# Performance work log

Measured on AMD Instinct MI355X. Metric: run time of the kernel, lower is better.

## Reference

```python
import jax, jax.numpy as jnp
import numpy as np

SEQ, SUB, B, V = 32, 16, 512, 258
U = SEQ // SUB
Z, CH, CO, DH = 512, 1024, 512, 1024


def _lstm_cell(x, h, c, Wi, Wh, bi, bh):
    # torch gate order: input, forget, cell, output
    g = x @ Wi + h @ Wh + bi + bh  # [B, 4H]
    i, f, gg, o = jnp.split(g, 4, axis=-1)
    c = jax.nn.sigmoid(f) * c + jax.nn.sigmoid(i) * jnp.tanh(gg)
    h = jax.nn.sigmoid(o) * jnp.tanh(c)
    return h, c


def _lstm2(xs, h1_0, p1, p2):
    # xs: [T,B,in]; h1_0: [B,H] layer-1 initial hidden.
    # Layer-2 hidden and both cell states start at zero (initialize_state in torch code).
    z0 = jnp.zeros_like(h1_0)
    def step(carry, x):
        h1, c1, h2, c2 = carry
        h1, c1 = _lstm_cell(x, h1, c1, *p1)
        h2, c2 = _lstm_cell(h1, h2, c2, *p2)
        return (h1, c1, h2, c2), h2
    _, hs = jax.lax.scan(step, (h1_0, z0, z0, z0), xs)
    return hs  # [T,B,H] top-layer hidden states


def setup_inputs() -> dict:
    key = jax.random.key(0)
    ks = iter(jax.random.split(key, 40))
    def w(shape, s=0.05):
        return jax.random.normal(next(ks), shape, dtype=jnp.float32) * s
    return {
        "z": jax.random.normal(next(ks), (B, Z), dtype=jnp.float32),
        "x": jax.random.uniform(next(ks), (SEQ, B, V), dtype=jnp.float32),
        "conductor_input": w((1, B, V)),
        "ci_W": w((Z, CH)), "ci_b": w((CH,)),
        "cW1i": w((V, 4 * CH)), "cW1h": w((CH, 4 * CH)), "cb1i": w((4 * CH,)), "cb1h": w((4 * CH,)),
        "cW2i": w((CH, 4 * CH)), "cW2h": w((CH, 4 * CH)), "cb2i": w((4 * CH,)), "cb2h": w((4 * CH,)),
        "co_W": w((CH, CO)), "co_b": w((CO,)),
        "di_W": w((CO, DH)), "di_b": w((DH,)),
        "dW1i": w((CO + V, 4 * DH)), "dW1h": w((DH, 4 * DH)), "db1i": w((4 * DH,)), "db1h": w((4 * DH,)),
        "dW2i": w((DH, 4 * DH)), "dW2h": w((DH, 4 * DH)), "db2i": w((4 * DH,)), "db2h": w((4 * DH,)),
        "fc_W": w((DH, V)), "fc_b": w((V,)),
    }


def reference(z, x, conductor_input, ci_W, ci_b, cW1i, cW1h, cb1i, cb1h, cW2i, cW2h, cb2i, cb2h, co_W, co_b, di_W, di_b, dW1i, dW1h, db1i, db1h, dW2i, dW2h, db2i, db2h, fc_W, fc_b):
    # --- conductor: 2-layer LSTM over U steps of a learned constant input ---
    h1 = jnp.tanh(z @ ci_W + ci_b)  # [B,CH] layer-1 init hidden
    cin = jnp.broadcast_to(conductor_input, (U, B, V))
    ch = _lstm2(cin, h1, (cW1i, cW1h, cb1i, cb1h), (cW2i, cW2h, cb2i, cb2h))  # [U,B,CH]
    c = ch @ co_W + co_b  # [U,B,CO]
    # --- decoder (teacher forcing): state resets each sub-sequence, so the U
    # segments of length SUB are independent given c -> vmap over segments ---
    sos = jnp.zeros((1, B, V), jnp.float32).at[:, :, 0].set(1.0)
    prev = jnp.concatenate([sos, x[:-1]], axis=0).reshape(U, SUB, B, V)
    cb = jnp.broadcast_to(c[:, None], (U, SUB, B, CO))
    dec_in = jnp.concatenate([cb, prev], axis=-1)  # [U,SUB,B,CO+V]
    def run_seg(xs, cj):
        h1_0 = jnp.tanh(cj @ di_W + di_b)  # [B,DH]
        return _lstm2(xs, h1_0, (dW1i, dW1h, db1i, db1h), (dW2i, dW2h, db2i, db2h))
    hs = jax.vmap(run_seg)(dec_in, c)  # [U,SUB,B,DH]
    logp = jax.nn.log_softmax(hs @ fc_W + fc_b, axis=-1)  # log(softmax(.)) fused
    return logp.reshape(SEQ, B, V).transpose(1, 0, 2)  # [B,SEQ,V]
```

## Files before the change

kernel.cpp:

```cpp
#include <hip/hip_runtime.h>
#include <cstddef>
#include <cstdint>


namespace {

typedef short s8v __attribute__((ext_vector_type(8)));
typedef float f4v __attribute__((ext_vector_type(4)));
typedef unsigned short ushort_t;

__device__ inline unsigned short f2bf(float f) {
    union { float f; unsigned u; } v; v.f = f;
    unsigned r = v.u + 0x7fff + ((v.u >> 16) & 1);
    return (unsigned short)(r >> 16);
}
__device__ inline float bf2f(ushort_t u) {
    union { unsigned u; float f; } v; v.u = ((unsigned)u) << 16; return v.f;
}
__device__ inline float sigm_f(float x) { return 1.f / (1.f + __expf(-x)); }
__device__ inline float tanh_f(float x) {
    const float e = __expf(2.f * fabsf(x));
    return copysignf(1.f - 2.f / (e + 1.f), x);
}

#define GLOAD_LDS(gp, lp)                                              \
    __builtin_amdgcn_global_load_lds(                                  \
        (const __attribute__((address_space(1))) void*)(gp),           \
        (__attribute__((address_space(3))) void*)(lp), 16, 0, 0)

__device__ __forceinline__ void gemm_core(
    const ushort_t* __restrict__ A1a, const ushort_t* __restrict__ A1b,
    int lda1, int K1, const ushort_t* __restrict__ B1t,
    const ushort_t* __restrict__ A2, int lda2, int K2,
    const ushort_t* __restrict__ B2t,
    int bm, int bn, ushort_t* lds, f4v acc[4][4])
{
    const int tid = threadIdx.x;
    const int wid = tid >> 6;
    const int lane = tid & 63;

    const int sr0 = wid * 16 + (lane >> 2);
    const int sr1 = sr0 + 64;
    const int rl0 = sr0 ^ ((sr0 >> 2) & 1);
    const int rl1 = sr1 ^ ((sr1 >> 2) & 1);
    const int c0 = (((lane & 3) ^ (rl0 & 3)) << 3);
    const int c1 = (((lane & 3) ^ (rl1 & 3)) << 3);
    const int ldst = wid * 512;

    auto arow = [&](const ushort_t* Aa, const ushort_t* Ab, int lda,
                    int r) -> const ushort_t* {
        return (Ab != nullptr && r >= 512) ? Ab + (size_t)(r - 512) * lda
                                           : Aa + (size_t)r * lda;
    };
    const ushort_t* a0 = arow(A1a, A1b, lda1, bm + rl0) + c0;
    const ushort_t* a1 = arow(A1a, A1b, lda1, bm + rl1) + c1;
    const ushort_t* b0 = B1t + (size_t)(bn + rl0) * K1 + c0;
    const ushort_t* b1 = B1t + (size_t)(bn + rl1) * K1 + c1;

    auto stage = [&](int buf) {
        ushort_t* Lb = lds + buf * 8192;
        GLOAD_LDS(a0, Lb + ldst);
        GLOAD_LDS(a1, Lb + 2048 + ldst);
        GLOAD_LDS(b0, Lb + 4096 + ldst);
        GLOAD_LDS(b1, Lb + 6144 + ldst);
        a0 += 32; a1 += 32; b0 += 32; b1 += 32;
    };

    const int wr = wid >> 1, wc = wid & 1;
    const int lrow = lane & 15, lkg = lane >> 4;
    int aoff[4], boff[4];
#pragma unroll
    for (int m = 0; m < 4; ++m) {
        const int r = wr * 64 + m * 16 + lrow;
        aoff[m] = (r ^ ((r >> 2) & 1)) * 32 + ((lkg ^ (r & 3)) << 3);
    }
#pragma unroll
    for (int n = 0; n < 4; ++n) {
        const int r = wc * 64 + n * 16 + lrow;
        boff[n] = 4096 + (r ^ ((r >> 2) & 1)) * 32 + ((lkg ^ (r & 3)) << 3);
    }

    auto compute = [&](int buf) {
        const ushort_t* L = lds + buf * 8192;
        s8v af[4], bv[4];
#pragma unroll
        for (int m = 0; m < 4; ++m) af[m] = *(const s8v*)(L + aoff[m]);
#pragma unroll
        for (int n = 0; n < 4; ++n) bv[n] = *(const s8v*)(L + boff[n]);
#pragma unroll
        for (int m = 0; m < 4; ++m)
#pragma unroll
            for (int n = 0; n < 4; ++n)
                acc[m][n] = __builtin_amdgcn_mfma_f32_16x16x32_bf16(
                    af[m], bv[n], acc[m][n], 0, 0, 0);
    };

    const int n1 = K1 >> 5, n2 = K2 >> 5;
    stage(0);
    __syncthreads();
    int cur = 0;
    for (int t = 0; t < n1; ++t) {
        if (t + 1 < n1) {
            stage(cur ^ 1);
        } else if (n2 > 0) {
            a0 = A2 + (size_t)(bm + rl0) * lda2 + c0;
            a1 = A2 + (size_t)(bm + rl1) * lda2 + c1;
            b0 = B2t + (size_t)(bn + rl0) * K2 + c0;
            b1 = B2t + (size_t)(bn + rl1) * K2 + c1;
            stage(cur ^ 1);
        }
        compute(cur);
        __syncthreads();
        cur ^= 1;
    }
    for (int t = 0; t < n2; ++t) {
        if (t + 1 < n2) stage(cur ^ 1);
        compute(cur);
        __syncthreads();
        cur ^= 1;
    }
}

template <int ACT>
__global__ __launch_bounds__(256) void plain_gemm(
    const ushort_t* __restrict__ A, int lda, int K,
    const ushort_t* __restrict__ Bt,
    const float* __restrict__ bias, int bias_n,
    float* __restrict__ C, ushort_t* __restrict__ Cbf, int N)
{
    __shared__ __align__(16) ushort_t lds[2 * 8192];
    const int bm = blockIdx.x * 128, bn = blockIdx.y * 128;
    f4v acc[4][4] = {};
    gemm_core(A, nullptr, lda, K, Bt, nullptr, 0, 0, nullptr, bm, bn, lds, acc);

    const int tid = threadIdx.x, wid = tid >> 6, lane = tid & 63;
    const int wr = wid >> 1, wc = wid & 1, lrow = lane & 15, lkg = lane >> 4;
#pragma unroll
    for (int m = 0; m < 4; ++m) {
        const int row0 = bm + wr * 64 + m * 16 + lkg * 4;
#pragma unroll
        for (int n = 0; n < 4; ++n) {
            const int col = bn + wc * 64 + n * 16 + lrow;
            const float bv = (bias != nullptr && col < bias_n) ? bias[col] : 0.f;
#pragma unroll
            for (int r = 0; r < 4; ++r) {
                float v = acc[m][n][r] + bv;
                if (ACT == 1) v = tanh_f(v);
                const size_t o = (size_t)(row0 + r) * N + col;
                if (C != nullptr) C[o] = v;
                if (Cbf != nullptr) Cbf[o] = f2bf(v);
            }
        }
    }
}

struct Prob {
    const ushort_t* A1a; const ushort_t* A1b; int lda1; int K1;
    const ushort_t* B1t;
    const ushort_t* A2; int lda2; int K2; const ushort_t* B2t;
    const ushort_t* Dbf;
    const float* bias;
    float* cst;
    ushort_t* hout;
    ushort_t* hs;
    int step_s;
};

__global__ __launch_bounds__(256) void lstm_step(Prob PA, int nxa, Prob PB,
                                                 int mshift)
{
    __shared__ __align__(16) ushort_t lds[2 * 8192];
    const int nblk = gridDim.x;
    const int wg = blockIdx.x;
    const int swz = (wg & 7) * (nblk >> 3) + (wg >> 3);
    const int nmb = 1 << mshift;
    const int nb = swz >> mshift;
    const int mb = swz & (nmb - 1);

    const bool isA = mb < nxa;
    const Prob& P = isA ? PA : PB;
    const int bm = (isA ? mb : mb - nxa) * 128;
    const int bn = nb * 128;

    f4v acc[4][4] = {};
    gemm_core(P.A1a, P.A1b, P.lda1, P.K1, P.B1t,
              P.A2, P.lda2, P.K2, P.B2t, bm, bn, lds, acc);

    const int tid = threadIdx.x, wid = tid >> 6, lane = tid & 63;
    const int wr = wid >> 1, wc = wid & 1, lrow = lane & 15, lkg = lane >> 4;
    const int colbase = bn + wc * 64;
    const int jb = (colbase >> 6) * 16 + lrow;

#pragma unroll
    for (int m = 0; m < 4; ++m) {
        const int row0 = bm + wr * 64 + m * 16 + lkg * 4;
#pragma unroll
        for (int r = 0; r < 4; ++r) {
            const int row = row0 + r;
            float g0 = acc[m][0][r], g1 = acc[m][1][r];
            float g2 = acc[m][2][r], g3 = acc[m][3][r];
            if (P.Dbf != nullptr) {
                const ushort_t* d = P.Dbf + (size_t)row * 4096 + colbase + lrow;
                g0 += bf2f(d[0]); g1 += bf2f(d[16]);
                g2 += bf2f(d[32]); g3 += bf2f(d[48]);
            }
            if (P.bias != nullptr) {
                const float* b = P.bias + colbase + lrow;
                g0 += b[0]; g1 += b[16]; g2 += b[32]; g3 += b[48];
            }
            const size_t ci = (size_t)row * 1024 + jb;
            const float cn = fmaf(sigm_f(g1), P.cst[ci], sigm_f(g0) * tanh_f(g2));
            const float hn = sigm_f(g3) * tanh_f(cn);
            P.cst[ci] = cn;
            const ushort_t hb = f2bf(hn);
            P.hout[ci] = hb;
            if (P.hs != nullptr) {
                size_t d;
                if (P.step_s >= 0) {
                    const int u = row >> 9, b = row & 511;
                    d = ((size_t)((u * 16 + P.step_s) * 512 + b) << 10) + jb;
                } else {
                    d = ci;
                }
                P.hs[d] = hb;
            }
        }
    }
}

template <int PERM>
__global__ __launch_bounds__(256) void transpose_to_bf16(
    const float* __restrict__ in, ushort_t* __restrict__ out,
    int K, int N, int Kp, int Np)
{
    __shared__ float tile[32][33];
    const int k0 = blockIdx.x * 32, n0 = blockIdx.y * 32;
    const int tx = threadIdx.x, ty = threadIdx.y;
#pragma unroll
    for (int q = 0; q < 4; ++q) {
        const int k = k0 + ty + 8 * q, n = n0 + tx;
        tile[ty + 8 * q][tx] = (k < K && n < N) ? in[(size_t)k * N + n] : 0.f;
    }
    __syncthreads();
#pragma unroll
    for (int q = 0; q < 4; ++q) {
        const int n = n0 + ty + 8 * q, k = k0 + tx;
        int np = n;
        if (PERM) np = ((n & 1023) >> 4) * 64 + (n >> 10) * 16 + (n & 15);
        out[(size_t)np * Kp + k] = f2bf(tile[tx][ty + 8 * q]);
    }
}

__global__ void convert_pad_bf16(const float* __restrict__ in,
                                 ushort_t* __restrict__ out,
                                 int K, int Kp, int total)
{
    const int idx = blockIdx.x * 256 + threadIdx.x;
    if (idx >= total) return;
    const int r = idx / Kp, k = idx - r * Kp;
    out[idx] = (k < K) ? f2bf(in[(size_t)r * K + k]) : (ushort_t)0;
}

__global__ void sos_init_bf16(ushort_t* __restrict__ sos)
{
    const int i = blockIdx.x * 256 + threadIdx.x;
    if (i < 512 * 288) sos[i] = ((i % 288) == 0) ? (ushort_t)0x3F80 : (ushort_t)0;
}

__global__ void permute_bias(const float* __restrict__ b1,
                             const float* __restrict__ b2,
                             float* __restrict__ out)
{
    const int c = blockIdx.x * 256 + threadIdx.x;
    if (c >= 4096) return;
    const int g = (c >> 4) & 3;
    const int j = (c >> 6) * 16 + (c & 15);
    out[c] = b1[g * 1024 + j] + b2[g * 1024 + j];
}

__global__ __launch_bounds__(256) void logsoftmax_kernel(
    const float* __restrict__ logits, float* __restrict__ out)
{
    const int row = blockIdx.x;
    const int tid = threadIdx.x;
    const float* L = logits + (size_t)row * 384;
    const int t = row >> 9;
    const int b = row & 511;
    float* O = out + ((size_t)b * 32 + t) * 258;

    const float x0 = L[tid];
    const float x1 = (tid < 2) ? L[256 + tid] : -1e30f;

    __shared__ float sm[4];
    float m = fmaxf(x0, x1);
#pragma unroll
    for (int off = 32; off > 0; off >>= 1) m = fmaxf(m, __shfl_down(m, off));
    if ((tid & 63) == 0) sm[tid >> 6] = m;
    __syncthreads();
    m = fmaxf(fmaxf(sm[0], sm[1]), fmaxf(sm[2], sm[3]));
    __syncthreads();

    float s = expf(x0 - m) + ((tid < 2) ? expf(x1 - m) : 0.f);
#pragma unroll
    for (int off = 32; off > 0; off >>= 1) s += __shfl_down(s, off);
    if ((tid & 63) == 0) sm[tid >> 6] = s;
    __syncthreads();
    s = sm[0] + sm[1] + sm[2] + sm[3];

    const float lse = m + logf(s);
    O[tid] = x0 - lse;
    if (tid < 2) O[256 + tid] = x1 - lse;
}

}

extern "C" void kernel_launch(void* const* d_in, const int* in_sizes, int n_in,
                              void* d_out, int out_size, void* d_ws, size_t ws_size,
                              hipStream_t stream)
{
    (void)in_sizes; (void)n_in; (void)out_size; (void)ws_size;

    const float* z    = (const float*)d_in[0];
    const float* x    = (const float*)d_in[1];
    const float* cin  = (const float*)d_in[2];
    const float* ciW  = (const float*)d_in[3];
    const float* cib  = (const float*)d_in[4];
    const float* cW1i = (const float*)d_in[5];
    const float* cW1h = (const float*)d_in[6];
    const float* cb1i = (const float*)d_in[7];
    const float* cb1h = (const float*)d_in[8];
    const float* cW2i = (const float*)d_in[9];
    const float* cW2h = (const float*)d_in[10];
    const float* cb2i = (const float*)d_in[11];
    const float* cb2h = (const float*)d_in[12];
    const float* coW  = (const float*)d_in[13];
    const float* cob  = (const float*)d_in[14];
    const float* diW  = (const float*)d_in[15];
    const float* dib  = (const float*)d_in[16];
    const float* dW1i = (const float*)d_in[17];
    const float* dW1h = (const float*)d_in[18];
    const float* db1i = (const float*)d_in[19];
    const float* db1h = (const float*)d_in[20];
    const float* dW2i = (const float*)d_in[21];
    const float* dW2h = (const float*)d_in[22];
    const float* db2i = (const float*)d_in[23];
    const float* db2h = (const float*)d_in[24];
    const float* fcW  = (const float*)d_in[25];
    const float* fcb  = (const float*)d_in[26];
    float* out = (float*)d_out;

    char* wsp = (char*)d_ws;
    size_t off = 0;
    auto allocf = [&](size_t n) { float* p = (float*)(wsp + off); off += n * 4; return p; };
    auto allocb = [&](size_t n) { ushort_t* p = (ushort_t*)(wsp + off); off += n * 2; return p; };

    float* cst = allocf((size_t)3 * 1024 * 1024 + 64);
    float* c1c = cst;
    float* c2c = cst + (size_t)512 * 1024;
    float* c1d = cst + (size_t)1024 * 1024;
    float* c2d = cst + (size_t)2 * 1024 * 1024;
    float* pb1c = allocf(4096);
    float* pb2c = allocf(4096);
    float* pb1d = allocf(4096);
    float* pb2d = allocf(4096);
    float* logits = allocf((size_t)16384 * 384);

    ushort_t* h2z  = allocb((size_t)2 * (512 + 1024) * 1024);
    ushort_t* hc2A = h2z;
    ushort_t* hc2B = h2z + (size_t)512 * 1024;
    ushort_t* h2dA = h2z + (size_t)2 * 512 * 1024;
    ushort_t* h2dB = h2z + (size_t)(2 * 512 + 1024) * 1024;

    ushort_t* hc1A = allocb((size_t)512 * 1024);
    ushort_t* hc1B = allocb((size_t)512 * 1024);
    ushort_t* h1dA = allocb((size_t)1024 * 1024);
    ushort_t* h1dB = allocb((size_t)1024 * 1024);

    ushort_t* zbf    = allocb((size_t)512 * 512);
    ushort_t* cinbf  = allocb((size_t)512 * 288);
    ushort_t* sosbf  = allocb((size_t)512 * 288);
    ushort_t* xbf    = allocb((size_t)16384 * 288);
    ushort_t* chbf   = allocb((size_t)1024 * 1024);
    ushort_t* ccode  = allocb((size_t)1024 * 512);
    ushort_t* cpre   = allocb((size_t)1024 * 4096);
    ushort_t* xW1c   = allocb((size_t)512 * 4096);
    ushort_t* hsbf   = allocb((size_t)16384 * 1024);

    ushort_t* ciWt  = allocb((size_t)1024 * 512);
    ushort_t* cW1it = allocb((size_t)4096 * 288);
    ushort_t* cW1ht = allocb((size_t)4096 * 1024);
    ushort_t* cW2it = allocb((size_t)4096 * 1024);
    ushort_t* cW2ht = allocb((size_t)4096 * 1024);
    ushort_t* coWt  = allocb((size_t)512 * 1024);
    ushort_t* dtopt = allocb((size_t)4096 * 512);
    ushort_t* dbott = allocb((size_t)4096 * 288);
    ushort_t* diWt  = allocb((size_t)1024 * 512);
    ushort_t* dW1ht = allocb((size_t)4096 * 1024);
    ushort_t* dW2it = allocb((size_t)4096 * 1024);
    ushort_t* dW2ht = allocb((size_t)4096 * 1024);
    ushort_t* fcWt  = allocb((size_t)384 * 1024);

    hipMemsetAsync(cst, 0, (size_t)3 * 1024 * 1024 * 4, stream);
    hipMemsetAsync(h2z, 0, (size_t)2 * (512 + 1024) * 1024 * 2, stream);

    auto transp = [&](const float* in, ushort_t* o, int K, int N, int Kp, int Np, int perm) {
        dim3 g(Kp / 32, Np / 32), b(32, 8);
        if (perm) transpose_to_bf16<1><<<g, b, 0, stream>>>(in, o, K, N, Kp, Np);
        else      transpose_to_bf16<0><<<g, b, 0, stream>>>(in, o, K, N, Kp, Np);
    };
    transp(ciW, ciWt, 512, 1024, 512, 1024, 0);
    transp(cW1i, cW1it, 258, 4096, 288, 4096, 1);
    transp(cW1h, cW1ht, 1024, 4096, 1024, 4096, 1);
    transp(cW2i, cW2it, 1024, 4096, 1024, 4096, 1);
    transp(cW2h, cW2ht, 1024, 4096, 1024, 4096, 1);
    transp(coW, coWt, 1024, 512, 1024, 512, 0);
    transp(dW1i, dtopt, 512, 4096, 512, 4096, 1);
    transp(dW1i + (size_t)512 * 4096, dbott, 258, 4096, 288, 4096, 1);
    transp(diW, diWt, 512, 1024, 512, 1024, 0);
    transp(dW1h, dW1ht, 1024, 4096, 1024, 4096, 1);
    transp(dW2i, dW2it, 1024, 4096, 1024, 4096, 1);
    transp(dW2h, dW2ht, 1024, 4096, 1024, 4096, 1);
    transp(fcW, fcWt, 1024, 258, 1024, 384, 0);

    auto convert = [&](const float* in, ushort_t* o, int K, int Kp, int R) {
        const int total = R * Kp;
        convert_pad_bf16<<<dim3((total + 255) / 256), 256, 0, stream>>>(in, o, K, Kp, total);
    };
    convert(z, zbf, 512, 512, 512);
    convert(cin, cinbf, 258, 288, 512);
    convert(x, xbf, 258, 288, 16384);
    sos_init_bf16<<<dim3((512 * 288 + 255) / 256), 256, 0, stream>>>(sosbf);
    permute_bias<<<16, 256, 0, stream>>>(cb1i, cb1h, pb1c);
    permute_bias<<<16, 256, 0, stream>>>(cb2i, cb2h, pb2c);
    permute_bias<<<16, 256, 0, stream>>>(db1i, db1h, pb1d);
    permute_bias<<<16, 256, 0, stream>>>(db2i, db2h, pb2d);

    auto gemm = [&](int act, const ushort_t* A, int lda, int K, const ushort_t* Bt,
                    const float* bias, int bias_n,
                    float* C, ushort_t* Cbf, int M, int N) {
        dim3 g(M / 128, N / 128);
        if (act) plain_gemm<1><<<g, 256, 0, stream>>>(A, lda, K, Bt, bias, bias_n, C, Cbf, N);
        else     plain_gemm<0><<<g, 256, 0, stream>>>(A, lda, K, Bt, bias, bias_n, C, Cbf, N);
    };

    gemm(1, zbf, 512, 512, ciWt, cib, 1024, nullptr, hc1A, 512, 1024);
    gemm(0, cinbf, 288, 288, cW1it, pb1c, 4096, nullptr, xW1c, 512, 4096);

    ushort_t* HC1[2] = {hc1A, hc1B};
    ushort_t* HC2[2] = {hc2A, hc2B};
    for (int k = 0; k <= 2; ++k) {
        Prob pa{}, pb{};
        int nxa = 0, nxb = 0;
        if (k < 2) {
            pa = {HC1[k & 1], nullptr, 1024, 1024, cW1ht,
                  nullptr, 0, 0, nullptr,
                  xW1c, nullptr, c1c, HC1[(k + 1) & 1], nullptr, -1};
            nxa = 4;
        }
        if (k >= 1) {
            pb = {HC1[k & 1], nullptr, 1024, 1024, cW2it,
                  HC2[k & 1], 1024, 1024, cW2ht,
                  nullptr, pb2c, c2c, HC2[(k + 1) & 1],
                  chbf + (size_t)(k - 1) * 512 * 1024, -1};
            nxb = 4;
        }
        const int nmb = nxa + nxb;
        const int mshift = (nmb == 4) ? 2 : 3;
        lstm_step<<<dim3(nmb * 32), 256, 0, stream>>>(pa, nxa, pb, mshift);
    }

    gemm(0, chbf, 1024, 1024, coWt, cob, 512, nullptr, ccode, 1024, 512);
    gemm(0, ccode, 512, 512, dtopt, pb1d, 4096, nullptr, cpre, 1024, 4096);
    gemm(1, ccode, 512, 512, diWt, dib, 1024, nullptr, h1dA, 1024, 1024);

    ushort_t* H1[2] = {h1dA, h1dB};
    ushort_t* H2[2] = {h2dA, h2dB};
    for (int k = 0; k <= 16; ++k) {
        Prob pa{}, pb{};
        int nxa = 0, nxb = 0;
        if (k < 16) {
            const ushort_t* plo = (k == 0) ? sosbf : (xbf + (size_t)(k - 1) * 512 * 288);
            const ushort_t* phi = xbf + (size_t)(15 + k) * 512 * 288;
            pa = {plo, phi, 288, 288, dbott,
                  H1[k & 1], 1024, 1024, dW1ht,
                  cpre, nullptr, c1d, H1[(k + 1) & 1], nullptr, -1};
            nxa = 8;
        }
        if (k >= 1) {
            pb = {H1[k & 1], nullptr, 1024, 1024, dW2it,
                  H2[k & 1], 1024, 1024, dW2ht,
                  nullptr, pb2d, c2d, H2[(k + 1) & 1], hsbf, k - 1};
            nxb = 8;
        }
        const int nmb = nxa + nxb;
        const int mshift = (nmb == 8) ? 3 : 4;
        lstm_step<<<dim3(nmb * 32), 256, 0, stream>>>(pa, nxa, pb, mshift);
    }

    gemm(0, hsbf, 1024, 1024, fcWt, fcb, 258, logits, nullptr, 16384, 384);
    logsoftmax_kernel<<<dim3(16384), 256, 0, stream>>>(logits, out);
}
```

Baseline: 1.143 ms.

## Triple-buffer LDS in GEMM core with explicit vmcnt waits and MFMA priority

```diff
diff --git a/kernel.cpp b/kernel.cpp
--- a/kernel.cpp
+++ b/kernel.cpp
@@ -52,18 +52,35 @@
         return (Ab != nullptr && r >= 512) ? Ab + (size_t)(r - 512) * lda
                                            : Aa + (size_t)r * lda;
     };
-    const ushort_t* a0 = arow(A1a, A1b, lda1, bm + rl0) + c0;
-    const ushort_t* a1 = arow(A1a, A1b, lda1, bm + rl1) + c1;
-    const ushort_t* b0 = B1t + (size_t)(bn + rl0) * K1 + c0;
-    const ushort_t* b1 = B1t + (size_t)(bn + rl1) * K1 + c1;
-
-    auto stage = [&](int buf) {
+    const ushort_t* a1r0 = arow(A1a, A1b, lda1, bm + rl0) + c0;
+    const ushort_t* a1r1 = arow(A1a, A1b, lda1, bm + rl1) + c1;
+    const ushort_t* b1r0 = B1t + (size_t)(bn + rl0) * K1 + c0;
+    const ushort_t* b1r1 = B1t + (size_t)(bn + rl1) * K1 + c1;
+    const int n1 = K1 >> 5, n2 = (B2t != nullptr) ? (K2 >> 5) : 0;
+    const int nt = n1 + n2;
+    const ushort_t* a2r0 = nullptr; const ushort_t* a2r1 = nullptr;
+    const ushort_t* b2r0 = nullptr; const ushort_t* b2r1 = nullptr;
+    if (n2 > 0) {
+        a2r0 = A2 + (size_t)(bm + rl0) * lda2 + c0;
+        a2r1 = A2 + (size_t)(bm + rl1) * lda2 + c1;
+        b2r0 = B2t + (size_t)(bn + rl0) * K2 + c0;
+        b2r1 = B2t + (size_t)(bn + rl1) * K2 + c1;
+    }
+
+    auto stage = [&](int idx, int buf) {
         ushort_t* Lb = lds + buf * 8192;
-        GLOAD_LDS(a0, Lb + ldst);
-        GLOAD_LDS(a1, Lb + 2048 + ldst);
-        GLOAD_LDS(b0, Lb + 4096 + ldst);
-        GLOAD_LDS(b1, Lb + 6144 + ldst);
-        a0 += 32; a1 += 32; b0 += 32; b1 += 32;
+        const ushort_t *pa0, *pa1, *pb0, *pb1;
+        if (idx < n1) {
+            const int k0 = idx << 5;
+            pa0 = a1r0 + k0; pa1 = a1r1 + k0; pb0 = b1r0 + k0; pb1 = b1r1 + k0;
+        } else {
+            const int k0 = (idx - n1) << 5;
+            pa0 = a2r0 + k0; pa1 = a2r1 + k0; pb0 = b2r0 + k0; pb1 = b2r1 + k0;
+        }
+        GLOAD_LDS(pa0, Lb + ldst);
+        GLOAD_LDS(pa1, Lb + 2048 + ldst);
+        GLOAD_LDS(pb0, Lb + 4096 + ldst);
+        GLOAD_LDS(pb1, Lb + 6144 + ldst);
     };
 
     const int wr = wid >> 1, wc = wid & 1;
@@ -80,44 +97,36 @@
         boff[n] = 4096 + (r ^ ((r >> 2) & 1)) * 32 + ((lkg ^ (r & 3)) << 3);
     }
 
-    auto compute = [&](int buf) {
-        const ushort_t* L = lds + buf * 8192;
+    stage(0, 0);
+    stage(1, 1);
+    int sbuf = 2, cbuf = 0;
+    for (int t = 0; t < nt; ++t) {
+        if (t == nt - 1) {
+            asm volatile("s_waitcnt vmcnt(0)" ::: "memory");
+        } else {
+            asm volatile("s_waitcnt vmcnt(4)" ::: "memory");
+        }
+        __builtin_amdgcn_s_barrier();
+        __builtin_amdgcn_sched_barrier(0);
+        if (t + 2 < nt) {
+            stage(t + 2, sbuf);
+            sbuf = (sbuf == 2) ? 0 : sbuf + 1;
+        }
+        const ushort_t* L = lds + cbuf * 8192;
         s8v af[4], bv[4];
 #pragma unroll
         for (int m = 0; m < 4; ++m) af[m] = *(const s8v*)(L + aoff[m]);
 #pragma unroll
         for (int n = 0; n < 4; ++n) bv[n] = *(const s8v*)(L + boff[n]);
+        __builtin_amdgcn_s_setprio(1);
 #pragma unroll
         for (int m = 0; m < 4; ++m)
 #pragma unroll
             for (int n = 0; n < 4; ++n)
                 acc[m][n] = __builtin_amdgcn_mfma_f32_16x16x32_bf16(
                     af[m], bv[n], acc[m][n], 0, 0, 0);
-    };
-
-    const int n1 = K1 >> 5, n2 = K2 >> 5;
-    stage(0);
-    __syncthreads();
-    int cur = 0;
-    for (int t = 0; t < n1; ++t) {
-        if (t + 1 < n1) {
-            stage(cur ^ 1);
-        } else if (n2 > 0) {
-            a0 = A2 + (size_t)(bm + rl0) * lda2 + c0;
-            a1 = A2 + (size_t)(bm + rl1) * lda2 + c1;
-            b0 = B2t + (size_t)(bn + rl0) * K2 + c0;
-            b1 = B2t + (size_t)(bn + rl1) * K2 + c1;
-            stage(cur ^ 1);
-        }
-        compute(cur);
-        __syncthreads();
-        cur ^= 1;
-    }
-    for (int t = 0; t < n2; ++t) {
-        if (t + 1 < n2) stage(cur ^ 1);
-        compute(cur);
-        __syncthreads();
-        cur ^= 1;
+        __builtin_amdgcn_s_setprio(0);
+        cbuf = (cbuf == 2) ? 0 : cbuf + 1;
     }
 }
 
@@ -128,7 +137,7 @@
     const float* __restrict__ bias, int bias_n,
     float* __restrict__ C, ushort_t* __restrict__ Cbf, int N)
 {
-    __shared__ __align__(16) ushort_t lds[2 * 8192];
+    __shared__ __align__(16) ushort_t lds[3 * 8192];
     const int bm = blockIdx.x * 128, bn = blockIdx.y * 128;
     f4v acc[4][4] = {};
     gemm_core(A, nullptr, lda, K, Bt, nullptr, 0, 0, nullptr, bm, bn, lds, acc);
@@ -169,7 +178,7 @@
 __global__ __launch_bounds__(256) void lstm_step(Prob PA, int nxa, Prob PB,
                                                  int mshift)
 {
-    __shared__ __align__(16) ushort_t lds[2 * 8192];
+    __shared__ __align__(16) ushort_t lds[3 * 8192];
     const int nblk = gridDim.x;
     const int wg = blockIdx.x;
     const int swz = (wg & 7) * (nblk >> 3) + (wg >> 3);
```

Result: faster. 1.108 ms (-3.0%).
